# Kernel optimization log

Hardware: AMD Instinct MI355X
Metric: run time of the kernel (lower is better)

The kernel has to match this reference:

```python
import jax, jax.numpy as jnp
import numpy as np

B, T, D, H, C = 256, 512, 128, 256, 10


def gru_layer(x, Wih, Whh, bih, bhh):
    # x: [B,T,Din]; Wih: [3H,Din]; Whh: [3H,H]; biases: [3H]
    # PyTorch gate order: r, z, n
    gi = jnp.einsum('btd,gd->btg', x, Wih) + bih  # [B,T,3H] input part, precomputed
    gi = jnp.transpose(gi, (1, 0, 2))             # [T,B,3H] for scan

    def step(h, gi_t):
        gh = h @ Whh.T + bhh                      # [B,3H]
        r = jax.nn.sigmoid(gi_t[:, :H] + gh[:, :H])
        z = jax.nn.sigmoid(gi_t[:, H:2 * H] + gh[:, H:2 * H])
        n = jnp.tanh(gi_t[:, 2 * H:] + r * gh[:, 2 * H:])
        h_new = (1.0 - z) * n + z * h
        return h_new, h_new

    h0 = jnp.zeros((x.shape[0], H), dtype=x.dtype)
    _, hs = jax.lax.scan(step, h0, gi)            # hs: [T,B,H]
    return jnp.transpose(hs, (1, 0, 2))           # [B,T,H]


def setup_inputs() -> dict:
    key = jax.random.key(0)
    ks = jax.random.split(key, 12)
    s_in = 1.0 / np.sqrt(H)
    inp = {
        'x': jax.random.normal(ks[0], (B, T, D), dtype=jnp.float32),
        'Wih0': jax.random.uniform(ks[1], (3 * H, D), jnp.float32, -s_in, s_in),
        'Whh0': jax.random.uniform(ks[2], (3 * H, H), jnp.float32, -s_in, s_in),
        'bih0': jax.random.uniform(ks[3], (3 * H,), jnp.float32, -s_in, s_in),
        'bhh0': jax.random.uniform(ks[4], (3 * H,), jnp.float32, -s_in, s_in),
        'Wih1': jax.random.uniform(ks[5], (3 * H, H), jnp.float32, -s_in, s_in),
        'Whh1': jax.random.uniform(ks[6], (3 * H, H), jnp.float32, -s_in, s_in),
        'bih1': jax.random.uniform(ks[7], (3 * H,), jnp.float32, -s_in, s_in),
        'bhh1': jax.random.uniform(ks[8], (3 * H,), jnp.float32, -s_in, s_in),
        'Wfc': jax.random.uniform(ks[9], (C, H), jnp.float32, -s_in, s_in),
        'bfc': jax.random.uniform(ks[10], (C,), jnp.float32, -s_in, s_in),
    }
    return inp


def reference(x, Wih0, Whh0, bih0, bhh0, Wih1, Whh1, bih1, bhh1, Wfc, bfc):
    h1 = gru_layer(x, Wih0, Whh0, bih0, bhh0)     # [B,T,H]
    h2 = gru_layer(h1, Wih1, Whh1, bih1, bhh1)    # [B,T,H]
    last = h2[:, -1, :]                           # [B,H] last timestep
    return last @ Wfc.T + bfc                     # [B,C]
```

## Files before the change

kernel.cpp:

```cpp
#include <hip/hip_runtime.h>
#include <hip/hip_fp16.h>
#include <cstddef>
#include <cstdint>

#define B_  256
#define T_  512
#define D_  128
#define H_  256
#define G3_ 768
#define C_  10

typedef _Float16 f16x8 __attribute__((ext_vector_type(8)));
typedef float    f32x4 __attribute__((ext_vector_type(4)));

__device__ __forceinline__ float sigmoid_f(float x) {
    return 1.0f / (1.0f + __expf(-x));
}
__device__ __forceinline__ float tanh_f(float x) {
    return 1.0f - 2.0f / (__expf(2.0f * x) + 1.0f);
}

__device__ __forceinline__ unsigned int packh2(float a, float b) {
    unsigned short lo = __half_as_ushort(__float2half(a));
    unsigned short hi = __half_as_ushort(__float2half(b));
    return (unsigned int)lo | ((unsigned int)hi << 16);
}

__global__ void k_pack_whh(const float* __restrict__ Whh, uint4* __restrict__ Wl) {
    const int wnt = blockIdx.x;
    const int w  = wnt / 6;
    const int nt = wnt % 6;
    const int t  = threadIdx.x;
    const int kt = t >> 6;
    const int l  = t & 63;
    const int g  = nt >> 1;
    const int n  = g * 256 + w * 32 + (nt & 1) * 16 + (l & 15);
    const int k0 = kt * 32 + (l >> 4) * 8;
    const float* row = Whh + (size_t)n * H_ + k0;
    uint4 u;
    u.x = packh2(row[0], row[1]);
    u.y = packh2(row[2], row[3]);
    u.z = packh2(row[4], row[5]);
    u.w = packh2(row[6], row[7]);
    Wl[(size_t)wnt * 512 + t] = u;
}

__global__ void k_pack_wih(const float* __restrict__ W, uint4* __restrict__ Wp,
                           int K) {
    const int KT = K >> 5;
    const int f  = blockIdx.x * 4 + (threadIdx.x >> 6);
    const int l  = threadIdx.x & 63;
    const int ntile = f / KT;
    const int kt    = f - ntile * KT;
    const int n  = ntile * 16 + (l & 15);
    const int k0 = kt * 32 + (l >> 4) * 8;
    const float* row = W + (size_t)n * K + k0;
    uint4 u;
    u.x = packh2(row[0], row[1]);
    u.y = packh2(row[2], row[3]);
    u.z = packh2(row[4], row[5]);
    u.w = packh2(row[6], row[7]);
    Wp[(size_t)f * 64 + l] = u;
}

__global__ __launch_bounds__(256) void k_gemm_f16(
    const float* __restrict__ A, long Abstride, int tcShift,
    const uint4* __restrict__ Wp,
    const float* __restrict__ bias, float* __restrict__ C,
    int K)
{
    const int tid = threadIdx.x;
    const int w  = tid >> 6;
    const int l  = tid & 63;
    const int c  = l & 15;
    const int g4 = l >> 4;
    const int m0 = blockIdx.y * 128;
    const int n0 = blockIdx.x * 64;
    const int KT = K >> 5;
    const int mask = (1 << tcShift) - 1;

    const float* Arow0;
    const float* Arow1;
    {
        int mg0 = m0 + w * 32 + c;
        int mg1 = mg0 + 16;
        Arow0 = A + (size_t)(mg0 >> tcShift) * Abstride + (size_t)(mg0 & mask) * K + g4 * 8;
        Arow1 = A + (size_t)(mg1 >> tcShift) * Abstride + (size_t)(mg1 & mask) * K + g4 * 8;
    }
    const uint4* Wb = Wp + (size_t)((n0 >> 4) * KT) * 64 + l;

    f32x4 acc[2][4] = {};

    for (int kt = 0; kt < KT; kt++) {
        f16x8 a0, a1;
        {
            float4 lo = *(const float4*)(Arow0 + kt * 32);
            float4 hi = *(const float4*)(Arow0 + kt * 32 + 4);
            a0[0] = (_Float16)lo.x; a0[1] = (_Float16)lo.y;
            a0[2] = (_Float16)lo.z; a0[3] = (_Float16)lo.w;
            a0[4] = (_Float16)hi.x; a0[5] = (_Float16)hi.y;
            a0[6] = (_Float16)hi.z; a0[7] = (_Float16)hi.w;
        }
        {
            float4 lo = *(const float4*)(Arow1 + kt * 32);
            float4 hi = *(const float4*)(Arow1 + kt * 32 + 4);
            a1[0] = (_Float16)lo.x; a1[1] = (_Float16)lo.y;
            a1[2] = (_Float16)lo.z; a1[3] = (_Float16)lo.w;
            a1[4] = (_Float16)hi.x; a1[5] = (_Float16)hi.y;
            a1[6] = (_Float16)hi.z; a1[7] = (_Float16)hi.w;
        }
#pragma unroll
        for (int ct = 0; ct < 4; ct++) {
            uint4 wf = Wb[(size_t)(ct * KT + kt) * 64];
            acc[0][ct] = __builtin_amdgcn_mfma_f32_16x16x32_f16(
                a0, __builtin_bit_cast(f16x8, wf), acc[0][ct], 0, 0, 0);
            acc[1][ct] = __builtin_amdgcn_mfma_f32_16x16x32_f16(
                a1, __builtin_bit_cast(f16x8, wf), acc[1][ct], 0, 0, 0);
        }
    }

#pragma unroll
    for (int ct = 0; ct < 4; ct++) {
        const int n = n0 + ct * 16 + c;
        const float bv = bias[n];
#pragma unroll
        for (int rt = 0; rt < 2; rt++) {
#pragma unroll
            for (int rg = 0; rg < 4; rg++) {
                const int m = m0 + w * 32 + rt * 16 + g4 * 4 + rg;
                C[(size_t)m * G3_ + n] = acc[rt][ct][rg] + bv;
            }
        }
    }
}

__device__ __forceinline__ void gru_scan_core(
    const float* __restrict__ gi,
    const uint4* __restrict__ Wpk,
    const float* __restrict__ bhh,
    float* __restrict__ h_state,
    float* __restrict__ out_seq,
    int Tc, int initZero,
    uint4 (&lds_w)[8192], _Float16 (&lds_h)[2][16][264])
{
    const int tid = threadIdx.x;
    const int w  = tid >> 6;
    const int l  = tid & 63;
    const int c  = l & 15;
    const int g4 = l >> 4;

#pragma unroll
    for (int i = 0; i < 16; i++) {
        int idx = i * 512 + tid;
        lds_w[idx] = Wpk[(size_t)(idx >> 10) * 3072 + 2048 + (idx & 1023)];
    }

    uint4 wreg[32];
#pragma unroll
    for (int nt = 0; nt < 4; nt++)
#pragma unroll
        for (int kt = 0; kt < 8; kt++)
            wreg[nt * 8 + kt] = Wpk[(size_t)((w * 6 + nt) * 8 + kt) * 64 + l];

    const int jA = w * 32 + c;
    const float br0 = bhh[jA],       br1 = bhh[jA + 16];
    const float bz0 = bhh[256 + jA], bz1 = bhh[256 + jA + 16];
    const float bn0 = bhh[512 + jA], bn1 = bhh[512 + jA + 16];

    float hreg[4][2];
#pragma unroll
    for (int r = 0; r < 4; r++) {
        const int m = g4 * 4 + r;
        if (initZero) {
            hreg[r][0] = 0.0f;
            hreg[r][1] = 0.0f;
        } else {
            hreg[r][0] = h_state[(size_t)m * H_ + jA];
            hreg[r][1] = h_state[(size_t)m * H_ + jA + 16];
        }
        lds_h[0][m][jA]      = (_Float16)hreg[r][0];
        lds_h[0][m][jA + 16] = (_Float16)hreg[r][1];
    }
    __syncthreads();

    int cur = 0;
    for (int tt = 0; tt < Tc; ++tt) {
        unsigned wb = (unsigned)(w * 1024 + l);
        asm volatile("" : "+v"(wb));

        float gic[4][6];
#pragma unroll
        for (int r = 0; r < 4; r++) {
            const float* gp = gi + ((size_t)(g4 * 4 + r) * Tc + tt) * G3_ + jA;
#pragma unroll
            for (int gg = 0; gg < 3; gg++) {
                gic[r][gg * 2 + 0] = gp[gg * 256];
                gic[r][gg * 2 + 1] = gp[gg * 256 + 16];
            }
        }

        f32x4 acc[6] = {};
#pragma unroll
        for (int kt = 0; kt < 8; kt++) {
            f16x8 a = *(const f16x8*)&lds_h[cur][c][kt * 32 + g4 * 8];
#pragma unroll
            for (int nt = 0; nt < 4; nt++)
                acc[nt] = __builtin_amdgcn_mfma_f32_16x16x32_f16(
                    a, __builtin_bit_cast(f16x8, wreg[nt * 8 + kt]), acc[nt], 0, 0, 0);
            uint4 u4 = lds_w[wb + kt * 64];
            acc[4] = __builtin_amdgcn_mfma_f32_16x16x32_f16(
                a, __builtin_bit_cast(f16x8, u4), acc[4], 0, 0, 0);
            uint4 u5 = lds_w[wb + (8 + kt) * 64];
            acc[5] = __builtin_amdgcn_mfma_f32_16x16x32_f16(
                a, __builtin_bit_cast(f16x8, u5), acc[5], 0, 0, 0);
        }

#pragma unroll
        for (int r = 0; r < 4; r++) {
            const int m = g4 * 4 + r;
#pragma unroll
            for (int jj = 0; jj < 2; jj++) {
                float rg = sigmoid_f(gic[r][jj]     + acc[jj][r]     + (jj ? br1 : br0));
                float zg = sigmoid_f(gic[r][2 + jj] + acc[2 + jj][r] + (jj ? bz1 : bz0));
                float ng = tanh_f(gic[r][4 + jj] +
                                  rg * (acc[4 + jj][r] + (jj ? bn1 : bn0)));
                float hn = (1.0f - zg) * ng + zg * hreg[r][jj];
                hreg[r][jj] = hn;
                lds_h[cur ^ 1][m][jA + jj * 16] = (_Float16)hn;
                if (out_seq)
                    out_seq[((size_t)m * Tc + tt) * H_ + jA + jj * 16] = hn;
            }
        }
        if (tt == Tc - 1) {
#pragma unroll
            for (int r = 0; r < 4; r++) {
                const int m = g4 * 4 + r;
                h_state[(size_t)m * H_ + jA]      = hreg[r][0];
                h_state[(size_t)m * H_ + jA + 16] = hreg[r][1];
            }
        }
        __syncthreads();
        cur ^= 1;
    }
}

__global__ __launch_bounds__(512, 2) void k_gru_scan_fused(
    const float* __restrict__ gi0, const uint4* __restrict__ wl0,
    const float* __restrict__ bhh0, float* __restrict__ hst0,
    float* __restrict__ h1c,
    const float* __restrict__ gi1, const uint4* __restrict__ wl1,
    const float* __restrict__ bhh1, float* __restrict__ hst1,
    int Tc, int do0, int do1, int init0, int init1)
{
    __shared__ __align__(16) uint4    lds_w[8192];
    __shared__ __align__(16) _Float16 lds_h[2][16][264];

    const int blk = blockIdx.x;
    if (blk < 16) {
        if (!do0) return;
        const int b0 = blk * 16;
        gru_scan_core(gi0 + (size_t)b0 * Tc * G3_, wl0, bhh0,
                      hst0 + (size_t)b0 * H_, h1c + (size_t)b0 * Tc * H_,
                      Tc, init0, lds_w, lds_h);
    } else {
        if (!do1) return;
        const int b0 = (blk - 16) * 16;
        gru_scan_core(gi1 + (size_t)b0 * Tc * G3_, wl1, bhh1,
                      hst1 + (size_t)b0 * H_, nullptr,
                      Tc, init1, lds_w, lds_h);
    }
}

__global__ void k_fc(const float* __restrict__ h, const float* __restrict__ Wfc,
                     const float* __restrict__ bfc, float* __restrict__ out)
{
    int idx = blockIdx.x * blockDim.x + threadIdx.x;
    if (idx >= B_ * C_) return;
    int b = idx / C_, c = idx % C_;
    const float* hp = h + (size_t)b * H_;
    const float* wp = Wfc + (size_t)c * H_;
    float s = bfc[c];
#pragma unroll 4
    for (int k = 0; k < H_; k++) s = fmaf(hp[k], wp[k], s);
    out[idx] = s;
}

extern "C" void kernel_launch(void* const* d_in, const int* in_sizes, int n_in,
                              void* d_out, int out_size, void* d_ws, size_t ws_size,
                              hipStream_t stream)
{
    const float* x    = (const float*)d_in[0];
    const float* Wih0 = (const float*)d_in[1];
    const float* Whh0 = (const float*)d_in[2];
    const float* bih0 = (const float*)d_in[3];
    const float* bhh0 = (const float*)d_in[4];
    const float* Wih1 = (const float*)d_in[5];
    const float* Whh1 = (const float*)d_in[6];
    const float* bih1 = (const float*)d_in[7];
    const float* bhh1 = (const float*)d_in[8];
    const float* Wfc  = (const float*)d_in[9];
    const float* bfc  = (const float*)d_in[10];
    float* out = (float*)d_out;

    const size_t wlBytes  = (size_t)48 * 512 * sizeof(uint4);
    const size_t wp0Bytes = (size_t)48 * 4 * 64 * sizeof(uint4);
    const size_t wp1Bytes = (size_t)48 * 8 * 64 * sizeof(uint4);

    const size_t fixedB = 2 * wlBytes + wp0Bytes + wp1Bytes
                        + 2 * (size_t)B_ * H_ * 4 + 16384;
    int Tc = 128, tcShift = 7;
    while (Tc > 1) {
        size_t need = fixedB
                    + 2 * (size_t)B_ * Tc * G3_ * 4
                    + (size_t)B_ * Tc * H_ * 4;
        if (need <= ws_size) break;
        Tc >>= 1; tcShift--;
    }
    const int nChunks = T_ / Tc;

    char* ws = (char*)d_ws;
    size_t off = 0;
    auto alloc = [&](size_t bytes) { char* p = ws + off; off += (bytes + 255) & ~(size_t)255; return p; };
    float* gi0  = (float*)alloc((size_t)B_ * Tc * G3_ * 4);
    float* gi1  = (float*)alloc((size_t)B_ * Tc * G3_ * 4);
    float* h1c  = (float*)alloc((size_t)B_ * Tc * H_ * 4);
    uint4* wl0  = (uint4*)alloc(wlBytes);
    uint4* wl1  = (uint4*)alloc(wlBytes);
    uint4* wp0  = (uint4*)alloc(wp0Bytes);
    uint4* wp1  = (uint4*)alloc(wp1Bytes);
    float* hst0 = (float*)alloc((size_t)B_ * H_ * 4);
    float* hst1 = (float*)alloc((size_t)B_ * H_ * 4);

    k_pack_whh<<<48, 512, 0, stream>>>(Whh0, wl0);
    k_pack_whh<<<48, 512, 0, stream>>>(Whh1, wl1);
    k_pack_wih<<<48, 256, 0, stream>>>(Wih0, wp0, D_);
    k_pack_wih<<<96, 256, 0, stream>>>(Wih1, wp1, H_);

    const dim3 ggrid(G3_ / 64, (B_ * Tc) / 128);

    k_gemm_f16<<<ggrid, 256, 0, stream>>>(
        x, (long)T_ * D_, tcShift, wp0, bih0, gi0, D_);
    k_gru_scan_fused<<<32, 512, 0, stream>>>(
        gi0, wl0, bhh0, hst0, h1c, gi1, wl1, bhh1, hst1,
        Tc, 1, 0, 1, 0);

    for (int c = 1; c < nChunks; ++c) {
        k_gemm_f16<<<ggrid, 256, 0, stream>>>(
            h1c, (long)Tc * H_, tcShift, wp1, bih1, gi1, H_);
        k_gemm_f16<<<ggrid, 256, 0, stream>>>(
            x + (size_t)c * Tc * D_, (long)T_ * D_, tcShift, wp0, bih0, gi0, D_);
        k_gru_scan_fused<<<32, 512, 0, stream>>>(
            gi0, wl0, bhh0, hst0, h1c, gi1, wl1, bhh1, hst1,
            Tc, 1, 1, 0, c == 1);
    }

    k_gemm_f16<<<ggrid, 256, 0, stream>>>(
        h1c, (long)Tc * H_, tcShift, wp1, bih1, gi1, H_);
    k_gru_scan_fused<<<32, 512, 0, stream>>>(
        gi0, wl0, bhh0, hst0, h1c, gi1, wl1, bhh1, hst1,
        Tc, 0, 1, 0, nChunks == 1);

    k_fc<<<10, 256, 0, stream>>>(hst1, Wfc, bfc, out);
}
```

Baseline: 2.407 ms.

## Split each GRU scan group across two blocks exchanging hidden halves via flags

Each batch-group's recurrent step is now split between two 256-thread blocks, each computing half of the hidden units. Every step the blocks swap their fp16 hidden halves through a global double-buffered exchange area, synchronised with per-block release/acquire flags. This halves the per-block matmul work and register/LDS weight load and doubles the number of active CUs. The cost is a cross-block spin-wait and global round trip on every timestep, and it depends on both partner blocks being co-resident.

```diff
diff --git a/kernel.cpp b/kernel.cpp
--- a/kernel.cpp
+++ b/kernel.cpp
@@ -140,7 +140,9 @@
     const float* __restrict__ bhh,
     float* __restrict__ h_state,
     float* __restrict__ out_seq,
-    int Tc, int initZero,
+    unsigned int* __restrict__ hx,
+    int* __restrict__ flags,
+    int blk, int par, int s, int Tc, int initZero, int base,
     uint4 (&lds_w)[8192], _Float16 (&lds_h)[2][16][264])
 {
     const int tid = threadIdx.x;
@@ -148,21 +150,29 @@
     const int l  = tid & 63;
     const int c  = l & 15;
     const int g4 = l >> 4;
-
-#pragma unroll
-    for (int i = 0; i < 16; i++) {
-        int idx = i * 512 + tid;
-        lds_w[idx] = Wpk[(size_t)(idx >> 10) * 3072 + 2048 + (idx & 1023)];
-    }
-
-    uint4 wreg[32];
-#pragma unroll
-    for (int nt = 0; nt < 4; nt++)
+    const int w8 = s * 4 + w;
+
+#pragma unroll
+    for (int i = 0; i < 32; i++) {
+        int idx = i * 256 + tid;
+        int set = idx >> 11;
+        int fi  = (idx >> 6) & 31;
+        int ln  = idx & 63;
+        int nt  = 2 + (fi >> 3);
+        int kt  = fi & 7;
+        lds_w[idx] = Wpk[(size_t)(((s * 4 + set) * 6 + nt) * 8 + kt) * 64 + ln];
+    }
+
+    f16x8 wreg[16];
+#pragma unroll
+    for (int nt = 0; nt < 2; nt++)
 #pragma unroll
         for (int kt = 0; kt < 8; kt++)
-            wreg[nt * 8 + kt] = Wpk[(size_t)((w * 6 + nt) * 8 + kt) * 64 + l];
-
-    const int jA = w * 32 + c;
+            wreg[nt * 8 + kt] = *reinterpret_cast<const f16x8*>(
+                Wpk + (size_t)((w8 * 6 + nt) * 8 + kt) * 64 + l);
+
+    const int jA  = s * 128 + w * 32 + c;
+    const int jAo = (s ^ 1) * 128 + w * 32 + c;
     const float br0 = bhh[jA],       br1 = bhh[jA + 16];
     const float bz0 = bhh[256 + jA], bz1 = bhh[256 + jA + 16];
     const float bn0 = bhh[512 + jA], bn1 = bhh[512 + jA + 16];
@@ -178,14 +188,33 @@
             hreg[r][0] = h_state[(size_t)m * H_ + jA];
             hreg[r][1] = h_state[(size_t)m * H_ + jA + 16];
         }
-        lds_h[0][m][jA]      = (_Float16)hreg[r][0];
-        lds_h[0][m][jA + 16] = (_Float16)hreg[r][1];
+    }
+    {
+        const int row = tid >> 4;
+        const int cc  = (tid & 15) * 16;
+        _Float16 tmp[16];
+        if (initZero) {
+#pragma unroll
+            for (int i = 0; i < 16; i++) tmp[i] = (_Float16)0.0f;
+        } else {
+            const float* hp = h_state + (size_t)row * H_ + cc;
+#pragma unroll
+            for (int i = 0; i < 16; i++) tmp[i] = (_Float16)hp[i];
+        }
+        *(uint4*)&lds_h[0][row][cc]     = *(const uint4*)&tmp[0];
+        *(uint4*)&lds_h[0][row][cc + 8] = *(const uint4*)&tmp[8];
     }
     __syncthreads();
 
     int cur = 0;
     for (int tt = 0; tt < Tc; ++tt) {
-        unsigned wb = (unsigned)(w * 1024 + l);
+        const int S = base + tt;
+        const bool lastStep = (tt == Tc - 1);
+
+#pragma unroll
+        for (int i = 0; i < 16; i++)
+            asm volatile("" : "+v"(wreg[i]));
+        unsigned wb = (unsigned)(w * 2048 + l);
         asm volatile("" : "+v"(wb));
 
         float gic[4][6];
@@ -199,25 +228,52 @@
             }
         }
 
+        if (tt > 0) {
+            if (tid == 0) {
+                int guard = 0;
+                while (__hip_atomic_load(&flags[par * 16], __ATOMIC_ACQUIRE,
+                                         __HIP_MEMORY_SCOPE_AGENT) < S &&
+                       guard < (1 << 20)) guard++;
+            }
+            __syncthreads();
+            const unsigned pb = ((unsigned)((S - 1) & 1) * 64 + (unsigned)par) * 16;
+            unsigned pv[4];
+#pragma unroll
+            for (int r = 0; r < 4; r++)
+                pv[r] = __hip_atomic_load(
+                    &hx[(pb + g4 * 4 + r) * 64 + w * 16 + c],
+                    __ATOMIC_RELAXED, __HIP_MEMORY_SCOPE_AGENT);
+#pragma unroll
+            for (int r = 0; r < 4; r++) {
+                const int m = g4 * 4 + r;
+                lds_h[cur][m][jAo] =
+                    __builtin_bit_cast(_Float16, (unsigned short)(pv[r] & 0xffffu));
+                lds_h[cur][m][jAo + 16] =
+                    __builtin_bit_cast(_Float16, (unsigned short)(pv[r] >> 16));
+            }
+        }
+        __syncthreads();
+
         f32x4 acc[6] = {};
 #pragma unroll
         for (int kt = 0; kt < 8; kt++) {
             f16x8 a = *(const f16x8*)&lds_h[cur][c][kt * 32 + g4 * 8];
-#pragma unroll
-            for (int nt = 0; nt < 4; nt++)
+            acc[0] = __builtin_amdgcn_mfma_f32_16x16x32_f16(
+                a, wreg[kt], acc[0], 0, 0, 0);
+            acc[1] = __builtin_amdgcn_mfma_f32_16x16x32_f16(
+                a, wreg[8 + kt], acc[1], 0, 0, 0);
+#pragma unroll
+            for (int nt = 2; nt < 6; nt++) {
+                uint4 u = lds_w[wb + ((nt - 2) * 8 + kt) * 64];
                 acc[nt] = __builtin_amdgcn_mfma_f32_16x16x32_f16(
-                    a, __builtin_bit_cast(f16x8, wreg[nt * 8 + kt]), acc[nt], 0, 0, 0);
-            uint4 u4 = lds_w[wb + kt * 64];
-            acc[4] = __builtin_amdgcn_mfma_f32_16x16x32_f16(
-                a, __builtin_bit_cast(f16x8, u4), acc[4], 0, 0, 0);
-            uint4 u5 = lds_w[wb + (8 + kt) * 64];
-            acc[5] = __builtin_amdgcn_mfma_f32_16x16x32_f16(
-                a, __builtin_bit_cast(f16x8, u5), acc[5], 0, 0, 0);
+                    a, __builtin_bit_cast(f16x8, u), acc[nt], 0, 0, 0);
+            }
         }
 
 #pragma unroll
         for (int r = 0; r < 4; r++) {
             const int m = g4 * 4 + r;
+            _Float16 q[2];
 #pragma unroll
             for (int jj = 0; jj < 2; jj++) {
                 float rg = sigmoid_f(gic[r][jj]     + acc[jj][r]     + (jj ? br1 : br0));
@@ -226,48 +282,68 @@
                                   rg * (acc[4 + jj][r] + (jj ? bn1 : bn0)));
                 float hn = (1.0f - zg) * ng + zg * hreg[r][jj];
                 hreg[r][jj] = hn;
-                lds_h[cur ^ 1][m][jA + jj * 16] = (_Float16)hn;
+                q[jj] = (_Float16)hn;
+                lds_h[cur ^ 1][m][jA + jj * 16] = q[jj];
                 if (out_seq)
                     out_seq[((size_t)m * Tc + tt) * H_ + jA + jj * 16] = hn;
             }
-        }
-        if (tt == Tc - 1) {
+            if (!lastStep) {
+                unsigned pk =
+                    (unsigned)__builtin_bit_cast(unsigned short, q[0]) |
+                    ((unsigned)__builtin_bit_cast(unsigned short, q[1]) << 16);
+                __hip_atomic_store(
+                    &hx[(((unsigned)(S & 1) * 64 + (unsigned)blk) * 16 + m) * 64 +
+                        w * 16 + c],
+                    pk, __ATOMIC_RELAXED, __HIP_MEMORY_SCOPE_AGENT);
+            }
+        }
+        if (lastStep) {
 #pragma unroll
             for (int r = 0; r < 4; r++) {
                 const int m = g4 * 4 + r;
                 h_state[(size_t)m * H_ + jA]      = hreg[r][0];
                 h_state[(size_t)m * H_ + jA + 16] = hreg[r][1];
             }
-        }
-        __syncthreads();
+        } else {
+            __threadfence();
+            __syncthreads();
+            if (tid == 0)
+                __hip_atomic_store(&flags[blk * 16], S + 1, __ATOMIC_RELEASE,
+                                   __HIP_MEMORY_SCOPE_AGENT);
+        }
         cur ^= 1;
     }
 }
 
-__global__ __launch_bounds__(512, 2) void k_gru_scan_fused(
+__global__ __launch_bounds__(256, 1) void k_gru_scan_fused(
     const float* __restrict__ gi0, const uint4* __restrict__ wl0,
     const float* __restrict__ bhh0, float* __restrict__ hst0,
     float* __restrict__ h1c,
     const float* __restrict__ gi1, const uint4* __restrict__ wl1,
     const float* __restrict__ bhh1, float* __restrict__ hst1,
-    int Tc, int do0, int do1, int init0, int init1)
+    unsigned int* __restrict__ hx, int* __restrict__ flags,
+    int Tc, int do0, int do1, int init0, int init1, int base0, int base1)
 {
     __shared__ __align__(16) uint4    lds_w[8192];
     __shared__ __align__(16) _Float16 lds_h[2][16][264];
 
     const int blk = blockIdx.x;
-    if (blk < 16) {
+    const int s   = blk >> 5;
+    const int grp = blk & 31;
+    const int par = blk ^ 32;
+    const int layer = grp >> 4;
+    const int b0 = (grp & 15) * 16;
+
+    if (layer == 0) {
         if (!do0) return;
-        const int b0 = blk * 16;
         gru_scan_core(gi0 + (size_t)b0 * Tc * G3_, wl0, bhh0,
                       hst0 + (size_t)b0 * H_, h1c + (size_t)b0 * Tc * H_,
-                      Tc, init0, lds_w, lds_h);
+                      hx, flags, blk, par, s, Tc, init0, base0, lds_w, lds_h);
     } else {
         if (!do1) return;
-        const int b0 = (blk - 16) * 16;
         gru_scan_core(gi1 + (size_t)b0 * Tc * G3_, wl1, bhh1,
                       hst1 + (size_t)b0 * H_, nullptr,
-                      Tc, init1, lds_w, lds_h);
+                      hx, flags, blk, par, s, Tc, init1, base1, lds_w, lds_h);
     }
 }
 
@@ -305,8 +381,10 @@
     const size_t wlBytes  = (size_t)48 * 512 * sizeof(uint4);
     const size_t wp0Bytes = (size_t)48 * 4 * 64 * sizeof(uint4);
     const size_t wp1Bytes = (size_t)48 * 8 * 64 * sizeof(uint4);
-
-    const size_t fixedB = 2 * wlBytes + wp0Bytes + wp1Bytes
+    const size_t hxBytes  = (size_t)2 * 64 * 16 * 64 * 4;
+    const size_t flBytes  = (size_t)64 * 16 * 4;
+
+    const size_t fixedB = 2 * wlBytes + wp0Bytes + wp1Bytes + hxBytes + flBytes
                         + 2 * (size_t)B_ * H_ * 4 + 16384;
     int Tc = 128, tcShift = 7;
     while (Tc > 1) {
@@ -330,6 +408,10 @@
     uint4* wp1  = (uint4*)alloc(wp1Bytes);
     float* hst0 = (float*)alloc((size_t)B_ * H_ * 4);
     float* hst1 = (float*)alloc((size_t)B_ * H_ * 4);
+    unsigned int* hx = (unsigned int*)alloc(hxBytes);
+    int* flags  = (int*)alloc(flBytes);
+
+    hipMemsetAsync(flags, 0, flBytes, stream);
 
     k_pack_whh<<<48, 512, 0, stream>>>(Whh0, wl0);
     k_pack_whh<<<48, 512, 0, stream>>>(Whh1, wl1);
@@ -340,25 +422,25 @@
 
     k_gemm_f16<<<ggrid, 256, 0, stream>>>(
         x, (long)T_ * D_, tcShift, wp0, bih0, gi0, D_);
-    k_gru_scan_fused<<<32, 512, 0, stream>>>(
-        gi0, wl0, bhh0, hst0, h1c, gi1, wl1, bhh1, hst1,
-        Tc, 1, 0, 1, 0);
+    k_gru_scan_fused<<<64, 256, 0, stream>>>(
+        gi0, wl0, bhh0, hst0, h1c, gi1, wl1, bhh1, hst1, hx, flags,
+        Tc, 1, 0, 1, 0, 0, 0);
 
     for (int c = 1; c < nChunks; ++c) {
         k_gemm_f16<<<ggrid, 256, 0, stream>>>(
             h1c, (long)Tc * H_, tcShift, wp1, bih1, gi1, H_);
         k_gemm_f16<<<ggrid, 256, 0, stream>>>(
             x + (size_t)c * Tc * D_, (long)T_ * D_, tcShift, wp0, bih0, gi0, D_);
-        k_gru_scan_fused<<<32, 512, 0, stream>>>(
-            gi0, wl0, bhh0, hst0, h1c, gi1, wl1, bhh1, hst1,
-            Tc, 1, 1, 0, c == 1);
+        k_gru_scan_fused<<<64, 256, 0, stream>>>(
+            gi0, wl0, bhh0, hst0, h1c, gi1, wl1, bhh1, hst1, hx, flags,
+            Tc, 1, 1, 0, c == 1, c * Tc, (c - 1) * Tc);
     }
 
     k_gemm_f16<<<ggrid, 256, 0, stream>>>(
         h1c, (long)Tc * H_, tcShift, wp1, bih1, gi1, H_);
-    k_gru_scan_fused<<<32, 512, 0, stream>>>(
-        gi0, wl0, bhh0, hst0, h1c, gi1, wl1, bhh1, hst1,
-        Tc, 0, 1, 0, nChunks == 1);
+    k_gru_scan_fused<<<64, 256, 0, stream>>>(
+        gi0, wl0, bhh0, hst0, h1c, gi1, wl1, bhh1, hst1, hx, flags,
+        Tc, 0, 1, 0, nChunks == 1, 0, (nChunks - 1) * Tc);
 
     k_fc<<<10, 256, 0, stream>>>(hst1, Wfc, bfc, out);
 }
```

Measured after the change: 5.035 ms. 2.09x slower.

## Reorder gi layout for vector loads and reload Whh from global each step

Applied to the files above, without the earlier changes.

The input-projection GEMM now writes gi in a permuted column order, so each scan thread's six gate values sit next to each other and load as three float2 reads instead of six scattered scalars. The 32 Whh fragments that were held in registers for the whole scan are now re-read from global memory (cache) every timestep. Per-row offsets are precomputed to simplify addressing. This frees many VGPRs for occupancy and scheduling, at the cost of extra cache traffic on the serial critical path each step.

```diff
diff --git a/kernel.cpp b/kernel.cpp
--- a/kernel.cpp
+++ b/kernel.cpp
@@ -123,12 +123,15 @@
     for (int ct = 0; ct < 4; ct++) {
         const int n = n0 + ct * 16 + c;
         const float bv = bias[n];
+        const int g = n >> 8;
+        const int j = n & 255;
+        const int sidx = (((j >> 5) * 16 + (j & 15)) * 3 + g) * 2 + ((j >> 4) & 1);
 #pragma unroll
         for (int rt = 0; rt < 2; rt++) {
 #pragma unroll
             for (int rg = 0; rg < 4; rg++) {
                 const int m = m0 + w * 32 + rt * 16 + g4 * 4 + rg;
-                C[(size_t)m * G3_ + n] = acc[rt][ct][rg] + bv;
+                C[(size_t)m * G3_ + sidx] = acc[rt][ct][rg] + bv;
             }
         }
     }
@@ -155,17 +158,19 @@
         lds_w[idx] = Wpk[(size_t)(idx >> 10) * 3072 + 2048 + (idx & 1023)];
     }
 
-    uint4 wreg[32];
-#pragma unroll
-    for (int nt = 0; nt < 4; nt++)
-#pragma unroll
-        for (int kt = 0; kt < 8; kt++)
-            wreg[nt * 8 + kt] = Wpk[(size_t)((w * 6 + nt) * 8 + kt) * 64 + l];
-
     const int jA = w * 32 + c;
     const float br0 = bhh[jA],       br1 = bhh[jA + 16];
     const float bz0 = bhh[256 + jA], bz1 = bhh[256 + jA + 16];
     const float bn0 = bhh[512 + jA], bn1 = bhh[512 + jA + 16];
+
+    int voff_gi[4], voff_os[4];
+#pragma unroll
+    for (int r = 0; r < 4; r++) {
+        const int m = g4 * 4 + r;
+        voff_gi[r] = m * Tc * G3_ + (w * 16 + c) * 6;
+        voff_os[r] = m * Tc * H_ + jA;
+    }
+    const uint4* wptr = Wpk + (size_t)(w * 6 * 8) * 64 + l;
 
     float hreg[4][2];
 #pragma unroll
@@ -185,20 +190,30 @@
 
     int cur = 0;
     for (int tt = 0; tt < Tc; ++tt) {
+        const uint4* wp = wptr;
+        asm volatile("" : "+v"(wp));
+        f16x8 wreg[32];
+#pragma unroll
+        for (int i = 0; i < 32; i++)
+            wreg[i] = *reinterpret_cast<const f16x8*>(wp + (size_t)i * 64);
+
+        const float* gstep = gi + (size_t)tt * G3_;
+        float2 vg[4][3];
+#pragma unroll
+        for (int r = 0; r < 4; r++) {
+            const float* gp = gstep + voff_gi[r];
+            vg[r][0] = *(const float2*)gp;
+            vg[r][1] = *(const float2*)(gp + 2);
+            vg[r][2] = *(const float2*)(gp + 4);
+        }
+
+#pragma unroll
+        for (int i = 0; i < 32; i++)
+            asm volatile("" : "+v"(wreg[i]));
+
         unsigned wb = (unsigned)(w * 1024 + l);
         asm volatile("" : "+v"(wb));
 
-        float gic[4][6];
-#pragma unroll
-        for (int r = 0; r < 4; r++) {
-            const float* gp = gi + ((size_t)(g4 * 4 + r) * Tc + tt) * G3_ + jA;
-#pragma unroll
-            for (int gg = 0; gg < 3; gg++) {
-                gic[r][gg * 2 + 0] = gp[gg * 256];
-                gic[r][gg * 2 + 1] = gp[gg * 256 + 16];
-            }
-        }
-
         f32x4 acc[6] = {};
 #pragma unroll
         for (int kt = 0; kt < 8; kt++) {
@@ -206,7 +221,7 @@
 #pragma unroll
             for (int nt = 0; nt < 4; nt++)
                 acc[nt] = __builtin_amdgcn_mfma_f32_16x16x32_f16(
-                    a, __builtin_bit_cast(f16x8, wreg[nt * 8 + kt]), acc[nt], 0, 0, 0);
+                    a, wreg[nt * 8 + kt], acc[nt], 0, 0, 0);
             uint4 u4 = lds_w[wb + kt * 64];
             acc[4] = __builtin_amdgcn_mfma_f32_16x16x32_f16(
                 a, __builtin_bit_cast(f16x8, u4), acc[4], 0, 0, 0);
@@ -215,20 +230,23 @@
                 a, __builtin_bit_cast(f16x8, u5), acc[5], 0, 0, 0);
         }
 
+        float* osb = out_seq ? out_seq + (size_t)tt * H_ : nullptr;
 #pragma unroll
         for (int r = 0; r < 4; r++) {
             const int m = g4 * 4 + r;
 #pragma unroll
             for (int jj = 0; jj < 2; jj++) {
-                float rg = sigmoid_f(gic[r][jj]     + acc[jj][r]     + (jj ? br1 : br0));
-                float zg = sigmoid_f(gic[r][2 + jj] + acc[2 + jj][r] + (jj ? bz1 : bz0));
-                float ng = tanh_f(gic[r][4 + jj] +
-                                  rg * (acc[4 + jj][r] + (jj ? bn1 : bn0)));
+                const float gr = jj ? vg[r][0].y : vg[r][0].x;
+                const float gz = jj ? vg[r][1].y : vg[r][1].x;
+                const float gn = jj ? vg[r][2].y : vg[r][2].x;
+                float rg = sigmoid_f(gr + acc[jj][r]     + (jj ? br1 : br0));
+                float zg = sigmoid_f(gz + acc[2 + jj][r] + (jj ? bz1 : bz0));
+                float ng = tanh_f(gn + rg * (acc[4 + jj][r] + (jj ? bn1 : bn0)));
                 float hn = (1.0f - zg) * ng + zg * hreg[r][jj];
                 hreg[r][jj] = hn;
                 lds_h[cur ^ 1][m][jA + jj * 16] = (_Float16)hn;
-                if (out_seq)
-                    out_seq[((size_t)m * Tc + tt) * H_ + jA + jj * 16] = hn;
+                if (osb)
+                    osb[voff_os[r] + jj * 16] = hn;
             }
         }
         if (tt == Tc - 1) {
```

New measurement: 3.584 ms. +48.9%, slower.
